# Kernel optimization log

Hardware: AMD Instinct MI355X
Metric: run time of the kernel (lower is better)

Reference implementation:

```python
import jax, jax.numpy as jnp
import numpy as np

N_HEAD = 12
D_HEAD = 64


def setup_inputs() -> dict:
    key = jax.random.key(0)
    ks = jax.random.split(key, 9)
    bs, seq, d_model = 4, 2048, 768
    sc = 1.0 / np.sqrt(d_model)
    return {
        "q": jax.random.normal(ks[0], (bs, seq, d_model), jnp.float32),
        "k": jax.random.normal(ks[1], (bs, seq, d_model), jnp.float32),
        "v": jax.random.normal(ks[2], (bs, seq, d_model), jnp.float32),
        "Wq": jax.random.normal(ks[3], (d_model, d_model), jnp.float32) * sc,
        "bq": jax.random.normal(ks[4], (d_model,), jnp.float32) * 0.01,
        "Wk": jax.random.normal(ks[5], (d_model, d_model), jnp.float32) * sc,
        "bk": jax.random.normal(ks[6], (d_model,), jnp.float32) * 0.01,
        "Wv": jax.random.normal(ks[7], (d_model, d_model), jnp.float32) * sc,
        "bv": jax.random.normal(ks[8], (d_model,), jnp.float32) * 0.01,
    }


def _split_heads(x):
    # [bs, seq, n_head*d_head] -> [bs, n_head, seq, d_head]
    bs, seq, _ = x.shape
    return x.reshape(bs, seq, N_HEAD, D_HEAD).transpose(0, 2, 1, 3)


def reference(q, k, v, Wq, bq, Wk, bk, Wv, bv):
    # Linear projections (torch Linear: x @ W.T + b)
    wq = _split_heads(q @ Wq.T + bq)
    wk = _split_heads(k @ Wk.T + bk)
    wv = _split_heads(v @ Wv.T + bv)
    # scale=False in defaults -> raw dot products, no mask, dropout is eval no-op
    scores = jnp.einsum("bhqd,bhkd->bhqk", wq, wk)  # [bs, h, S, S]
    probs = jax.nn.softmax(scores, axis=-1)
    attn_vec = jnp.einsum("bhqk,bhkd->bhqd", probs, wv)
    bs, _, seq, _ = attn_vec.shape
    # merge heads -> [bs, seq, n_head*d_head]
    return attn_vec.transpose(0, 2, 1, 3).reshape(bs, seq, N_HEAD * D_HEAD)
```

## Files before the change

### kernel.cpp

```cpp
#include <hip/hip_runtime.h>
#include <stdint.h>

typedef _Float16 half8  __attribute__((ext_vector_type(8)));
typedef _Float16 half4v __attribute__((ext_vector_type(4)));
typedef float    floatx4 __attribute__((ext_vector_type(4)));

#define LOG2E 1.44269504088896340736f

__device__ __forceinline__ void gl_lds16(const _Float16* g, _Float16* l) {
  __builtin_amdgcn_global_load_lds(
      (__attribute__((address_space(1))) void*)g,
      (__attribute__((address_space(3))) void*)l, 16, 0, 0);
}

__device__ __forceinline__ half4v pack4(float a, float b, float c, float d) {
  auto lo = __builtin_amdgcn_cvt_pkrtz(a, b);
  auto hi = __builtin_amdgcn_cvt_pkrtz(c, d);
  return half4v{static_cast<_Float16>(lo[0]), static_cast<_Float16>(lo[1]),
                static_cast<_Float16>(hi[0]), static_cast<_Float16>(hi[1])};
}


__device__ __forceinline__ void issue_panel(const float* __restrict__ P,
                                            int r0, int k0, int tid,
                                            float4& a0, float4& a1,
                                            float4& b0, float4& b1) {
  {
    int G = tid;
    int r = G >> 2, gl = G & 3;
    int g = gl ^ ((r >> 1) & 3);
    const float4* s = (const float4*)(P + (size_t)(r0 + r) * 768 + k0 + g * 8);
    a0 = s[0]; a1 = s[1];
  }
  {
    int G = 256 + tid;
    int r = G >> 2, gl = G & 3;
    int g = gl ^ ((r >> 1) & 3);
    const float4* s = (const float4*)(P + (size_t)(r0 + r) * 768 + k0 + g * 8);
    b0 = s[0]; b1 = s[1];
  }
}

__device__ __forceinline__ void write_panel(_Float16* sb, int tid,
                                            const float4& a0, const float4& a1,
                                            const float4& b0, const float4& b1) {
  half8 h0 = { (_Float16)a0.x, (_Float16)a0.y, (_Float16)a0.z, (_Float16)a0.w,
               (_Float16)a1.x, (_Float16)a1.y, (_Float16)a1.z, (_Float16)a1.w };
  *(half8*)(sb + tid * 8) = h0;
  half8 h1 = { (_Float16)b0.x, (_Float16)b0.y, (_Float16)b0.z, (_Float16)b0.w,
               (_Float16)b1.x, (_Float16)b1.y, (_Float16)b1.z, (_Float16)b1.w };
  *(half8*)(sb + (256 + tid) * 8) = h1;
}

template <int BUF>
__device__ __forceinline__ void gemm_body(
    int knext, const float* __restrict__ X, const float* __restrict__ W,
    _Float16* As, _Float16* Bs, int m0, int n0, int tid, int z,
    int wr, int wc, int qd, int col, floatx4 (&acc)[4][4])
{
  const bool pref = (knext < 768);
  float4 xa0, xa1, xb0, xb1, wa0, wa1, wb0, wb1;
  if (pref) {
    issue_panel(X, m0, knext, tid, xa0, xa1, xb0, xb1);
    issue_panel(W, n0, knext, tid, wa0, wa1, wb0, wb1);
  }

  half8 af[4], bf[4];
  #pragma unroll
  for (int t = 0; t < 4; ++t) {
    int ra = wr * 64 + t * 16 + col;
    af[t] = *(const half8*)(As + BUF * 4096 + ra * 32 + ((qd ^ ((ra >> 1) & 3)) * 8));
  }
  #pragma unroll
  for (int t = 0; t < 4; ++t) {
    int rb = wc * 64 + t * 16 + col;
    bf[t] = *(const half8*)(Bs + BUF * 4096 + rb * 32 + ((qd ^ ((rb >> 1) & 3)) * 8));
  }
  if (z == 2) {
    #pragma unroll
    for (int i = 0; i < 4; ++i)
      #pragma unroll
      for (int j = 0; j < 4; ++j)
        acc[i][j] = __builtin_amdgcn_mfma_f32_16x16x32_f16(af[i], bf[j], acc[i][j], 0, 0, 0);
  } else {
    #pragma unroll
    for (int i = 0; i < 4; ++i)
      #pragma unroll
      for (int j = 0; j < 4; ++j)
        acc[i][j] = __builtin_amdgcn_mfma_f32_16x16x32_f16(bf[j], af[i], acc[i][j], 0, 0, 0);
  }

  if (pref) {
    write_panel(As + (1 - BUF) * 4096, tid, xa0, xa1, xb0, xb1);
    write_panel(Bs + (1 - BUF) * 4096, tid, wa0, wa1, wb0, wb1);
  }
  __syncthreads();
}

__global__ __launch_bounds__(256, 2) void qkv_gemm(
    const float* __restrict__ qx, const float* __restrict__ kx, const float* __restrict__ vx,
    const float* __restrict__ Wqp, const float* __restrict__ Wkp, const float* __restrict__ Wvp,
    const float* __restrict__ bqp, const float* __restrict__ bkp, const float* __restrict__ bvp,
    _Float16* __restrict__ oq, _Float16* __restrict__ ok, _Float16* __restrict__ ovt)
{
  __shared__ __attribute__((aligned(16))) char smem[40960];
  _Float16* As = (_Float16*)smem;
  _Float16* Bs = (_Float16*)(smem + 16384);
  _Float16* Es = (_Float16*)smem;

  const int tid  = threadIdx.x;
  const int lane = tid & 63, wid = tid >> 6;
  const int wr = wid >> 1, wc = wid & 1;
  const int qd = lane >> 4, col = lane & 15;

  #pragma unroll 1
  for (int t = blockIdx.x; t < 1152; t += 512) {
    const int m0 = (t & 63) * 128;
    const int n0 = ((t >> 6) % 6) * 128;
    const int z  = t / 384;
    const float* X = (z == 0) ? qx : ((z == 1) ? kx : vx);
    const float* W = (z == 0) ? Wqp : ((z == 1) ? Wkp : Wvp);

    const floatx4 z4 = {0.f, 0.f, 0.f, 0.f};
    floatx4 acc[4][4];
    #pragma unroll
    for (int i = 0; i < 4; ++i)
      #pragma unroll
      for (int j = 0; j < 4; ++j) acc[i][j] = z4;

    {
      float4 xa0, xa1, xb0, xb1, wa0, wa1, wb0, wb1;
      issue_panel(X, m0, 0, tid, xa0, xa1, xb0, xb1);
      issue_panel(W, n0, 0, tid, wa0, wa1, wb0, wb1);
      __syncthreads();
      write_panel(As, tid, xa0, xa1, xb0, xb1);
      write_panel(Bs, tid, wa0, wa1, wb0, wb1);
    }
    __syncthreads();
    for (int kk = 0; kk < 768; kk += 64) {
      gemm_body<0>(kk + 32, X, W, As, Bs, m0, n0, tid, z, wr, wc, qd, col, acc);
      gemm_body<1>(kk + 64, X, W, As, Bs, m0, n0, tid, z, wr, wc, qd, col, acc);
    }

    const float* bias = (z == 0) ? bqp : ((z == 1) ? bkp : bvp);
    const int b = m0 >> 11, s0 = m0 & 2047;
    if (z == 2) {
      #pragma unroll
      for (int j = 0; j < 4; ++j) {
        int n_loc = wc * 64 + j * 16 + col;
        float bb = bias[n0 + n_loc];
        #pragma unroll
        for (int i = 0; i < 4; ++i) {
          int s_loc = wr * 64 + i * 16 + qd * 4;
          half4v h = pack4(acc[i][j][0] + bb, acc[i][j][1] + bb,
                           acc[i][j][2] + bb, acc[i][j][3] + bb);
          *(half4v*)(Es + n_loc * 160 + s_loc) = h;
        }
      }
      __syncthreads();
      #pragma unroll
      for (int it = 0; it < 8; ++it) {
        int row = it * 16 + (tid >> 4);
        int k   = tid & 15;
        half8 vr = *(const half8*)(Es + row * 160 + k * 8);
        *(half8*)(ovt + ((size_t)(b * 768 + n0 + row)) * 2048 + s0 + k * 8) = vr;
      }
    } else {
      _Float16* O = (z == 0) ? oq : ok;
      const float scale = (z == 0) ? LOG2E : 1.0f;
      #pragma unroll
      for (int j = 0; j < 4; ++j) {
        int n_loc = wc * 64 + j * 16 + qd * 4;
        float4 bb = *(const float4*)(bias + n0 + n_loc);
        #pragma unroll
        for (int i = 0; i < 4; ++i) {
          int s_loc = wr * 64 + i * 16 + col;
          half4v h = pack4((acc[i][j][0] + bb.x) * scale, (acc[i][j][1] + bb.y) * scale,
                           (acc[i][j][2] + bb.z) * scale, (acc[i][j][3] + bb.w) * scale);
          *(half4v*)(Es + s_loc * 160 + n_loc) = h;
        }
      }
      __syncthreads();
      const int hh0 = n0 >> 6;
      #pragma unroll
      for (int it = 0; it < 8; ++it) {
        int seg = it * 32 + (tid >> 3);
        int s = seg >> 1, hseg = seg & 1;
        int k = tid & 7;
        half8 vr = *(const half8*)(Es + s * 160 + hseg * 64 + k * 8);
        int mb = (m0 + s) >> 11, sg = (m0 + s) & 2047;
        *(half8*)(O + (size_t)(mb * 12 + hh0 + hseg) * 131072
                    + (size_t)sg * 64 + k * 8) = vr;
      }
    }
  }
}


__device__ __forceinline__ void stage_kv(const _Float16* __restrict__ Kg,
                                         const _Float16* __restrict__ Vg,
                                         _Float16* ksd, _Float16* vsd, int j0, int tid) {
  #pragma unroll
  for (int i = 0; i < 2; ++i) {
    int c = i * 256 + tid;
    int row = c >> 3, sc = c & 7;
    gl_lds16(Kg + (size_t)(j0 + row) * 64 + ((sc ^ (row & 7)) * 8), ksd + c * 8);
    gl_lds16(Vg + (size_t)row * 2048 + j0 + ((sc ^ (row & 7)) * 8), vsd + c * 8);
  }
}

template <int BUF>
__device__ __forceinline__ void attn_body(
    int jnext, const _Float16* __restrict__ Kg, const _Float16* __restrict__ Vg,
    _Float16* Ks, _Float16* Vs, int tid,
    const half8 (&qf)[2][2], int kb0, int kb1, const int (&vb)[4],
    floatx4 (&negm)[2], floatx4 (&ol)[2], floatx4 (&o)[4][2])
{
  if (jnext < 2048)
    stage_kv(Kg, Vg, Ks + (1 - BUF) * 4096, Vs + (1 - BUF) * 4096, jnext, tid);

  const char* ksb = (const char*)Ks;
  const char* vsb = (const char*)Vs;

  floatx4 st[4][2];
  #pragma unroll
  for (int t = 0; t < 4; ++t) {
    half8 kf0 = *(const half8*)(ksb + BUF * 8192 + t * 2048 + kb0);
    half8 kf1 = *(const half8*)(ksb + BUF * 8192 + t * 2048 + kb1);
    #pragma unroll
    for (int qt = 0; qt < 2; ++qt) {
      st[t][qt] = __builtin_amdgcn_mfma_f32_16x16x32_f16(kf0, qf[qt][0], negm[qt], 0, 0, 0);
      st[t][qt] = __builtin_amdgcn_mfma_f32_16x16x32_f16(kf1, qf[qt][1], st[t][qt], 0, 0, 0);
    }
  }

  float mr[2];
  #pragma unroll
  for (int qt = 0; qt < 2; ++qt) {
    float v = fmaxf(
        fmaxf(fmaxf(fmaxf(st[0][qt][0], st[0][qt][1]), fmaxf(st[0][qt][2], st[0][qt][3])),
              fmaxf(fmaxf(st[1][qt][0], st[1][qt][1]), fmaxf(st[1][qt][2], st[1][qt][3]))),
        fmaxf(fmaxf(fmaxf(st[2][qt][0], st[2][qt][1]), fmaxf(st[2][qt][2], st[2][qt][3])),
              fmaxf(fmaxf(st[3][qt][0], st[3][qt][1]), fmaxf(st[3][qt][2], st[3][qt][3]))));
    v = fmaxf(v, __shfl_xor(v, 16, 64));
    v = fmaxf(v, __shfl_xor(v, 32, 64));
    mr[qt] = fmaxf(v, 0.f);
  }

  half4v pf[4][2];
  #pragma unroll
  for (int qt = 0; qt < 2; ++qt)
    #pragma unroll
    for (int t = 0; t < 4; ++t)
      pf[t][qt] = pack4(__builtin_amdgcn_exp2f(st[t][qt][0] - mr[qt]),
                        __builtin_amdgcn_exp2f(st[t][qt][1] - mr[qt]),
                        __builtin_amdgcn_exp2f(st[t][qt][2] - mr[qt]),
                        __builtin_amdgcn_exp2f(st[t][qt][3] - mr[qt]));

  if (__any(mr[0] > 0.f || mr[1] > 0.f)) {
    #pragma unroll
    for (int qt = 0; qt < 2; ++qt) {
      float al = __builtin_amdgcn_exp2f(-mr[qt]);
      negm[qt] -= mr[qt];
      ol[qt] *= al;
      #pragma unroll
      for (int dt = 0; dt < 4; ++dt) o[dt][qt] *= al;
    }
  }

  const half4v vone = {(_Float16)1.0f, (_Float16)1.0f, (_Float16)1.0f, (_Float16)1.0f};
  #pragma unroll
  for (int dt = 0; dt < 4; ++dt) {
    #pragma unroll
    for (int t = 0; t < 4; ++t) {
      half4v vf = *(const half4v*)(vsb + BUF * 8192 + dt * 2048 + vb[t]);
      #pragma unroll
      for (int qt = 0; qt < 2; ++qt)
        o[dt][qt] = __builtin_amdgcn_mfma_f32_16x16x16f16(vf, pf[t][qt], o[dt][qt], 0, 0, 0);
    }
  }
  #pragma unroll
  for (int t = 0; t < 4; ++t)
    #pragma unroll
    for (int qt = 0; qt < 2; ++qt)
      ol[qt] = __builtin_amdgcn_mfma_f32_16x16x16f16(vone, pf[t][qt], ol[qt], 0, 0, 0);

  __syncthreads();
}

__global__ __launch_bounds__(256, 3) void attn_kernel(
    const _Float16* __restrict__ Qm,
    const _Float16* __restrict__ Km,
    const _Float16* __restrict__ Vt,
    float* __restrict__ out)
{
  __shared__ __attribute__((aligned(16))) _Float16 Ks[2 * 4096];
  __shared__ __attribute__((aligned(16))) _Float16 Vs[2 * 4096];
  const int bh = blockIdx.x;
  const int q0 = blockIdx.y * 128;
  const int tid = threadIdx.x, lane = tid & 63, w = tid >> 6;
  const int qd = lane >> 4, col = lane & 15, c7 = col & 7;
  const _Float16* Qg = Qm + (size_t)bh * 131072;
  const _Float16* Kg = Km + (size_t)bh * 131072;
  const _Float16* Vg = Vt + (size_t)bh * 131072;

  half8 qf[2][2];
  #pragma unroll
  for (int qt = 0; qt < 2; ++qt)
    #pragma unroll
    for (int ks = 0; ks < 2; ++ks)
      qf[qt][ks] = *(const half8*)(Qg + (size_t)(q0 + w * 32 + qt * 16 + col) * 64
                                   + (ks * 4 + qd) * 8);

  const int kb0 = col * 128 + ((qd ^ c7) * 16);
  const int kb1 = col * 128 + (((4 + qd) ^ c7) * 16);
  const int vq = (qd >> 1) ^ c7;
  int vb[4];
  #pragma unroll
  for (int t = 0; t < 4; ++t)
    vb[t] = col * 128 + (qd & 1) * 8 + ((vq ^ (2 * t)) * 16);

  floatx4 negm[2] = {{100.f, 100.f, 100.f, 100.f}, {100.f, 100.f, 100.f, 100.f}};
  const floatx4 z4 = {0.f, 0.f, 0.f, 0.f};
  floatx4 ol[2] = {z4, z4};
  floatx4 o[4][2];
  #pragma unroll
  for (int dt = 0; dt < 4; ++dt)
    #pragma unroll
    for (int qt = 0; qt < 2; ++qt) o[dt][qt] = z4;

  stage_kv(Kg, Vg, Ks, Vs, 0, tid);
  __syncthreads();

  for (int jj = 0; jj < 2048; jj += 128) {
    attn_body<0>(jj + 64,  Kg, Vg, Ks, Vs, tid, qf, kb0, kb1, vb, negm, ol, o);
    attn_body<1>(jj + 128, Kg, Vg, Ks, Vs, tid, qf, kb0, kb1, vb, negm, ol, o);
  }

  const int b = bh / 12, h = bh % 12;
  #pragma unroll
  for (int qt = 0; qt < 2; ++qt) {
    float inv = 1.0f / ol[qt][0];
    int qg = q0 + w * 32 + qt * 16 + col;
    float* obase = out + ((size_t)b * 2048 + qg) * 768 + h * 64;
    #pragma unroll
    for (int dt = 0; dt < 4; ++dt) {
      floatx4 v = o[dt][qt];
      v *= inv;
      *(floatx4*)(obase + dt * 16 + qd * 4) = v;
    }
  }
}

extern "C" void kernel_launch(void* const* d_in, const int* in_sizes, int n_in,
                              void* d_out, int out_size, void* d_ws, size_t ws_size,
                              hipStream_t stream) {
  const float* q  = (const float*)d_in[0];
  const float* k  = (const float*)d_in[1];
  const float* v  = (const float*)d_in[2];
  const float* Wq = (const float*)d_in[3];
  const float* bq = (const float*)d_in[4];
  const float* Wk = (const float*)d_in[5];
  const float* bk = (const float*)d_in[6];
  const float* Wv = (const float*)d_in[7];
  const float* bv = (const float*)d_in[8];

  const size_t NX = 6291456;
  const size_t need = 3 * NX * sizeof(_Float16);
  if (ws_size < need) return;

  _Float16* qh = (_Float16*)d_ws;
  _Float16* kh = qh + NX;
  _Float16* vt = kh + NX;

  qkv_gemm<<<dim3(512), 256, 0, stream>>>(q, k, v, Wq, Wk, Wv, bq, bk, bv, qh, kh, vt);
  attn_kernel<<<dim3(48, 16), 256, 0, stream>>>(qh, kh, vt, (float*)d_out);
}
```

Before: 273.4 us.

## Pre-convert inputs to fp16 and use direct-to-LDS triple-buffered QKV GEMM

Adds a conversion kernel that casts the q/k/v activations and the weights to fp16 in workspace. A new QKV GEMM then stages tiles with global_load_lds straight into a three-deep LDS ring, replacing register-staged fp32 loads, and launches a flat 3D grid instead of a persistent loop. This takes conversion and register staging out of the GEMM main loop, but it adds an extra pass that reads fp32 and writes fp16 over all inputs, plus one more kernel launch. The old fp32 path is kept as a fallback for when the workspace is too small.

```diff
diff --git a/kernel.cpp b/kernel.cpp
--- a/kernel.cpp
+++ b/kernel.cpp
@@ -18,6 +18,181 @@
   auto hi = __builtin_amdgcn_cvt_pkrtz(c, d);
   return half4v{static_cast<_Float16>(lo[0]), static_cast<_Float16>(lo[1]),
                 static_cast<_Float16>(hi[0]), static_cast<_Float16>(hi[1])};
+}
+
+struct CvtArgs {
+  const float* sx[3];
+  const float* sw[3];
+  _Float16*    dx;
+  _Float16*    dw;
+};
+
+__global__ void cvt_kernel(CvtArgs a) {
+  const int z  = blockIdx.y;
+  const int bx = blockIdx.x;
+  const float* src;
+  _Float16*    dst;
+  int base;
+  if (bx < 3072) { src = a.sx[z]; dst = a.dx + (size_t)z * 6291456; base = bx * 2048; }
+  else           { src = a.sw[z]; dst = a.dw + (size_t)z * 589824;  base = (bx - 3072) * 2048; }
+  const int i = base + threadIdx.x * 8;
+  const float4* s = (const float4*)(src + i);
+  float4 v0 = s[0], v1 = s[1];
+  half8 h = { (_Float16)v0.x, (_Float16)v0.y, (_Float16)v0.z, (_Float16)v0.w,
+              (_Float16)v1.x, (_Float16)v1.y, (_Float16)v1.z, (_Float16)v1.w };
+  *(half8*)(dst + i) = h;
+}
+
+
+__device__ __forceinline__ void gemm_stage16(const _Float16* __restrict__ P,
+                                             _Float16* sb, int r0, int k0, int tid) {
+  #pragma unroll
+  for (int i = 0; i < 2; ++i) {
+    int G = i * 256 + tid;
+    int r = G >> 2, gl = G & 3;
+    int g = gl ^ ((r >> 1) & 3);
+    gl_lds16(P + (size_t)(r0 + r) * 768 + k0 + g * 8, sb + G * 8);
+  }
+}
+
+template <int RB, int WB, int VM, bool PREF>
+__device__ __forceinline__ void gemm_body(
+    int kpre, const _Float16* __restrict__ X, const _Float16* __restrict__ W,
+    _Float16* As, _Float16* Bs, int m0, int n0, int tid, int z,
+    int wr, int wc, int qd, int col, floatx4 (&acc)[4][4])
+{
+  asm volatile("s_waitcnt vmcnt(%0)" :: "i"(VM) : "memory");
+  __builtin_amdgcn_s_barrier();
+  __builtin_amdgcn_sched_barrier(0);
+  if (PREF) {
+    gemm_stage16(X, As + WB * 4096, m0, kpre, tid);
+    gemm_stage16(W, Bs + WB * 4096, n0, kpre, tid);
+  }
+  __builtin_amdgcn_sched_barrier(0);
+
+  half8 af[4], bf[4];
+  #pragma unroll
+  for (int t = 0; t < 4; ++t) {
+    int ra = wr * 64 + t * 16 + col;
+    af[t] = *(const half8*)(As + RB * 4096 + ra * 32 + ((qd ^ ((ra >> 1) & 3)) * 8));
+  }
+  #pragma unroll
+  for (int t = 0; t < 4; ++t) {
+    int rb = wc * 64 + t * 16 + col;
+    bf[t] = *(const half8*)(Bs + RB * 4096 + rb * 32 + ((qd ^ ((rb >> 1) & 3)) * 8));
+  }
+  if (z == 2) {
+    #pragma unroll
+    for (int i = 0; i < 4; ++i)
+      #pragma unroll
+      for (int j = 0; j < 4; ++j)
+        acc[i][j] = __builtin_amdgcn_mfma_f32_16x16x32_f16(af[i], bf[j], acc[i][j], 0, 0, 0);
+  } else {
+    #pragma unroll
+    for (int i = 0; i < 4; ++i)
+      #pragma unroll
+      for (int j = 0; j < 4; ++j)
+        acc[i][j] = __builtin_amdgcn_mfma_f32_16x16x32_f16(bf[j], af[i], acc[i][j], 0, 0, 0);
+  }
+}
+
+__global__ __launch_bounds__(256, 2) void qkv_gemm(
+    const _Float16* __restrict__ xh,
+    const _Float16* __restrict__ wh,
+    const float* __restrict__ bqp, const float* __restrict__ bkp, const float* __restrict__ bvp,
+    _Float16* __restrict__ oq, _Float16* __restrict__ ok, _Float16* __restrict__ ovt)
+{
+  __shared__ __attribute__((aligned(16))) char smem[49152];
+  _Float16* As = (_Float16*)smem;
+  _Float16* Bs = (_Float16*)(smem + 24576);
+  _Float16* Es = (_Float16*)smem;
+
+  const int z  = blockIdx.z;
+  const _Float16* X = xh + (size_t)z * 6291456;
+  const _Float16* W = wh + (size_t)z * 589824;
+  const int m0 = blockIdx.x * 128, n0 = blockIdx.y * 128;
+  const int tid  = threadIdx.x;
+  const int lane = tid & 63, wid = tid >> 6;
+  const int wr = wid >> 1, wc = wid & 1;
+  const int qd = lane >> 4, col = lane & 15;
+
+  const floatx4 z4 = {0.f, 0.f, 0.f, 0.f};
+  floatx4 acc[4][4];
+  #pragma unroll
+  for (int i = 0; i < 4; ++i)
+    #pragma unroll
+    for (int j = 0; j < 4; ++j) acc[i][j] = z4;
+
+  gemm_stage16(X, As,        m0, 0,  tid);
+  gemm_stage16(W, Bs,        n0, 0,  tid);
+  gemm_stage16(X, As + 4096, m0, 32, tid);
+  gemm_stage16(W, Bs + 4096, n0, 32, tid);
+
+  int jn = 64;
+  #pragma unroll 1
+  for (int it = 0; it < 7; ++it) {
+    gemm_body<0, 2, 4, true>(jn,      X, W, As, Bs, m0, n0, tid, z, wr, wc, qd, col, acc);
+    gemm_body<1, 0, 4, true>(jn + 32, X, W, As, Bs, m0, n0, tid, z, wr, wc, qd, col, acc);
+    gemm_body<2, 1, 4, true>(jn + 64, X, W, As, Bs, m0, n0, tid, z, wr, wc, qd, col, acc);
+    jn += 96;
+  }
+  gemm_body<0, 2, 4, true >(736, X, W, As, Bs, m0, n0, tid, z, wr, wc, qd, col, acc);
+  gemm_body<1, 0, 4, false>(0,   X, W, As, Bs, m0, n0, tid, z, wr, wc, qd, col, acc);
+  gemm_body<2, 1, 0, false>(0,   X, W, As, Bs, m0, n0, tid, z, wr, wc, qd, col, acc);
+
+  __syncthreads();
+
+  const float* bias = (z == 0) ? bqp : ((z == 1) ? bkp : bvp);
+  const int b = m0 >> 11, s0 = m0 & 2047;
+  if (z == 2) {
+    #pragma unroll
+    for (int j = 0; j < 4; ++j) {
+      int n_loc = wc * 64 + j * 16 + col;
+      float bb = bias[n0 + n_loc];
+      #pragma unroll
+      for (int i = 0; i < 4; ++i) {
+        int s_loc = wr * 64 + i * 16 + qd * 4;
+        half4v h = pack4(acc[i][j][0] + bb, acc[i][j][1] + bb,
+                         acc[i][j][2] + bb, acc[i][j][3] + bb);
+        *(half4v*)(Es + n_loc * 160 + s_loc) = h;
+      }
+    }
+    __syncthreads();
+    #pragma unroll
+    for (int it = 0; it < 8; ++it) {
+      int row = it * 16 + (tid >> 4);
+      int k   = tid & 15;
+      half8 vr = *(const half8*)(Es + row * 160 + k * 8);
+      *(half8*)(ovt + ((size_t)(b * 768 + n0 + row)) * 2048 + s0 + k * 8) = vr;
+    }
+  } else {
+    _Float16* O = (z == 0) ? oq : ok;
+    const float scale = (z == 0) ? LOG2E : 1.0f;
+    #pragma unroll
+    for (int j = 0; j < 4; ++j) {
+      int n_loc = wc * 64 + j * 16 + qd * 4;
+      float4 bb = *(const float4*)(bias + n0 + n_loc);
+      #pragma unroll
+      for (int i = 0; i < 4; ++i) {
+        int s_loc = wr * 64 + i * 16 + col;
+        half4v h = pack4((acc[i][j][0] + bb.x) * scale, (acc[i][j][1] + bb.y) * scale,
+                         (acc[i][j][2] + bb.z) * scale, (acc[i][j][3] + bb.w) * scale);
+        *(half4v*)(Es + s_loc * 160 + n_loc) = h;
+      }
+    }
+    __syncthreads();
+    const int hh0 = n0 >> 6;
+    #pragma unroll
+    for (int it = 0; it < 8; ++it) {
+      int seg = it * 32 + (tid >> 3);
+      int s = seg >> 1, hseg = seg & 1;
+      int k = tid & 7;
+      half8 vr = *(const half8*)(Es + s * 160 + hseg * 64 + k * 8);
+      int mb = (m0 + s) >> 11, sg = (m0 + s) & 2047;
+      *(half8*)(O + (size_t)(mb * 12 + hh0 + hseg) * 131072
+                  + (size_t)sg * 64 + k * 8) = vr;
+    }
+  }
 }
 
 
@@ -53,7 +228,7 @@
 }
 
 template <int BUF>
-__device__ __forceinline__ void gemm_body(
+__device__ __forceinline__ void gemm_body_f32(
     int knext, const float* __restrict__ X, const float* __restrict__ W,
     _Float16* As, _Float16* Bs, int m0, int n0, int tid, int z,
     int wr, int wc, int qd, int col, floatx4 (&acc)[4][4])
@@ -97,7 +272,7 @@
   __syncthreads();
 }
 
-__global__ __launch_bounds__(256, 2) void qkv_gemm(
+__global__ __launch_bounds__(256, 2) void qkv_gemm_f32(
     const float* __restrict__ qx, const float* __restrict__ kx, const float* __restrict__ vx,
     const float* __restrict__ Wqp, const float* __restrict__ Wkp, const float* __restrict__ Wvp,
     const float* __restrict__ bqp, const float* __restrict__ bkp, const float* __restrict__ bvp,
@@ -138,8 +313,8 @@
     }
     __syncthreads();
     for (int kk = 0; kk < 768; kk += 64) {
-      gemm_body<0>(kk + 32, X, W, As, Bs, m0, n0, tid, z, wr, wc, qd, col, acc);
-      gemm_body<1>(kk + 64, X, W, As, Bs, m0, n0, tid, z, wr, wc, qd, col, acc);
+      gemm_body_f32<0>(kk + 32, X, W, As, Bs, m0, n0, tid, z, wr, wc, qd, col, acc);
+      gemm_body_f32<1>(kk + 64, X, W, As, Bs, m0, n0, tid, z, wr, wc, qd, col, acc);
     }
 
     const float* bias = (z == 0) ? bqp : ((z == 1) ? bkp : bvp);
@@ -366,13 +541,30 @@
   const float* bv = (const float*)d_in[8];
 
   const size_t NX = 6291456;
-  const size_t need = 3 * NX * sizeof(_Float16);
-  if (ws_size < need) return;
-
-  _Float16* qh = (_Float16*)d_ws;
-  _Float16* kh = qh + NX;
-  _Float16* vt = kh + NX;
-
-  qkv_gemm<<<dim3(512), 256, 0, stream>>>(q, k, v, Wq, Wk, Wv, bq, bk, bv, qh, kh, vt);
-  attn_kernel<<<dim3(48, 16), 256, 0, stream>>>(qh, kh, vt, (float*)d_out);
-}
+  const size_t NW = 589824;
+  const size_t need_full = (6 * NX + 3 * NW) * sizeof(_Float16);
+  const size_t need_min  = (3 * NX) * sizeof(_Float16);
+
+  if (ws_size >= need_full) {
+    _Float16* xh = (_Float16*)d_ws;
+    _Float16* wh = xh + 3 * NX;
+    _Float16* qh = wh + 3 * NW;
+    _Float16* kh = qh + NX;
+    _Float16* vt = kh + NX;
+
+    CvtArgs ca;
+    ca.sx[0] = q;  ca.sx[1] = k;  ca.sx[2] = v;
+    ca.sw[0] = Wq; ca.sw[1] = Wk; ca.sw[2] = Wv;
+    ca.dx = xh; ca.dw = wh;
+
+    cvt_kernel<<<dim3(3360, 3), 256, 0, stream>>>(ca);
+    qkv_gemm<<<dim3(64, 6, 3), 256, 0, stream>>>(xh, wh, bq, bk, bv, qh, kh, vt);
+    attn_kernel<<<dim3(48, 16), 256, 0, stream>>>(qh, kh, vt, (float*)d_out);
+  } else if (ws_size >= need_min) {
+    _Float16* qh = (_Float16*)d_ws;
+    _Float16* kh = qh + NX;
+    _Float16* vt = kh + NX;
+    qkv_gemm_f32<<<dim3(512), 256, 0, stream>>>(q, k, v, Wq, Wk, Wv, bq, bk, bv, qh, kh, vt);
+    attn_kernel<<<dim3(48, 16), 256, 0, stream>>>(qh, kh, vt, (float*)d_out);
+  }
+}
```

Result: faster. 247.3 us (median of 2 runs) (-9.6%).
